# Optimization experiments

Measured on AMD Instinct MI355X. Metric: run time of the kernel, lower is better.

Reference implementation:

```python
import jax, jax.numpy as jnp
import numpy as np

B, S, D_IN, D_HID, D_OUT, H = 2, 2048, 1024, 1024, 1024, 16
HD = D_HID // H  # head_dim = 64


def setup_inputs() -> dict:
    key = jax.random.key(0)
    ks = jax.random.split(key, 9)
    s_in = 1.0 / np.sqrt(D_IN)
    s_out = 1.0 / np.sqrt(D_OUT)
    return {
        "x": jax.random.normal(ks[0], (B, S, D_IN), dtype=jnp.float32),
        "Wq": jax.random.uniform(ks[1], (D_IN, D_HID), jnp.float32, -s_in, s_in),
        "bq": jax.random.uniform(ks[2], (D_HID,), jnp.float32, -s_in, s_in),
        "Wk": jax.random.uniform(ks[3], (D_IN, D_HID), jnp.float32, -s_in, s_in),
        "bk": jax.random.uniform(ks[4], (D_HID,), jnp.float32, -s_in, s_in),
        "Wv": jax.random.uniform(ks[5], (D_IN, D_OUT), jnp.float32, -s_in, s_in),
        "bv": jax.random.uniform(ks[6], (D_OUT,), jnp.float32, -s_in, s_in),
        "Wo": jax.random.uniform(ks[7], (D_OUT, D_OUT), jnp.float32, -s_out, s_out),
        "bo": jax.random.uniform(ks[8], (D_OUT,), jnp.float32, -s_out, s_out),
    }


def reference(x, Wq, bq, Wk, bk, Wv, bv, Wo, bo):
    b, s, _ = x.shape
    q = (x @ Wq + bq).reshape(b, s, H, HD)  # [B,S,H,HD]
    k = (x @ Wk + bk).reshape(b, s, H, HD)
    v = (x @ Wv + bv).reshape(b, s, H, HD)
    scores = jnp.einsum("bqhd,bkhd->bhqk", q, k) / jnp.sqrt(jnp.float32(HD))
    attn = jax.nn.softmax(scores, axis=-1)  # [B,H,S,S]
    ctx = jnp.einsum("bhqk,bkhd->bqhd", attn, v).reshape(b, s, D_HID)
    return ctx @ Wo + bo
```

## Files before the change

### kernel.cpp

```cpp
#include <hip/hip_runtime.h>
#include <stdint.h>

typedef __attribute__((ext_vector_type(8))) short short8v;
typedef __attribute__((ext_vector_type(4))) short short4v;
typedef __attribute__((ext_vector_type(4))) float float4v;
typedef __attribute__((ext_vector_type(4))) unsigned short ushort4v;
typedef __attribute__((ext_vector_type(4))) float floatvec4;
typedef __attribute__((ext_vector_type(2))) unsigned int uint2v;

#define DEVI __device__ __forceinline__

DEVI unsigned short f2bf(float f) {
    unsigned int u = __builtin_bit_cast(unsigned int, f);
    u += 0x7FFFu + ((u >> 16) & 1u);
    return (unsigned short)(u >> 16);
}

DEVI unsigned int pk2bf(float a, float b) {
#if defined(__has_builtin) && __has_builtin(__builtin_amdgcn_cvt_pk_bf16_f32)
    auto r = __builtin_amdgcn_cvt_pk_bf16_f32(a, b);
    unsigned int u;
    __builtin_memcpy(&u, &r, 4);
    return u;
#else
    return (unsigned int)f2bf(a) | ((unsigned int)f2bf(b) << 16);
#endif
}

DEVI float ex2(float x) {
#if defined(__has_builtin) && __has_builtin(__builtin_amdgcn_exp2f)
    return __builtin_amdgcn_exp2f(x);
#else
    return __builtin_exp2f(x);
#endif
}

typedef __attribute__((address_space(1))) void GV;
typedef __attribute__((address_space(3))) void LV;
DEVI void gl2lds16(const void* g, void* l) {
    __builtin_amdgcn_global_load_lds((GV*)g, (LV*)l, 16, 0, 0);
}

__global__ void conv_x_kernel(const float* __restrict__ x, unsigned short* __restrict__ xb) {
    const int i = (blockIdx.x * 256 + threadIdx.x) * 4;
    const floatvec4 v = *(const floatvec4*)&x[i];
    ushort4v o;
#pragma unroll
    for (int r = 0; r < 4; r++) o[r] = f2bf(v[r]);
    *(ushort4v*)&xb[i] = o;
}

__global__ void transpose_w4(const float* __restrict__ W0, const float* __restrict__ W1,
                             const float* __restrict__ W2, const float* __restrict__ W3,
                             unsigned short* __restrict__ D0, unsigned short* __restrict__ D1,
                             unsigned short* __restrict__ D2, unsigned short* __restrict__ D3) {
    __shared__ float t[32][33];
    const int tx = threadIdx.x, ty = threadIdx.y;
    const int bx = blockIdx.x, by = blockIdx.y, z = blockIdx.z;
    const float* W = (z == 0) ? W0 : (z == 1) ? W1 : (z == 2) ? W2 : W3;
    unsigned short* D = (z == 0) ? D0 : (z == 1) ? D1 : (z == 2) ? D2 : D3;
#pragma unroll
    for (int i = 0; i < 4; i++)
        t[ty + i * 8][tx] = W[(size_t)(by * 32 + ty + i * 8) * 1024 + bx * 32 + tx];
    __syncthreads();
#pragma unroll
    for (int i = 0; i < 4; i++)
        D[(size_t)(bx * 32 + ty + i * 8) * 1024 + by * 32 + tx] = f2bf(t[tx][ty + i * 8]);
}

__global__ __launch_bounds__(256, 2) void qkv_gemm(
    const unsigned short* __restrict__ X, const unsigned short* __restrict__ Wt,
    const float* __restrict__ bq, const float* __restrict__ bk, const float* __restrict__ bv,
    unsigned short* __restrict__ qb, unsigned short* __restrict__ kb,
    unsigned short* __restrict__ vtb)
{
    __shared__ __align__(16) unsigned short As[128 * 32];
    __shared__ __align__(16) unsigned short Bs[128 * 32];
    const int tid = threadIdx.x, lane = tid & 63, wv = tid >> 6;
    const int quad = lane >> 4, l16 = lane & 15;
    const int w = blockIdx.x >> 3;
    const int n0 = (blockIdx.x & 7) * 128;
    const int row0 = blockIdx.y * 128;
    const unsigned short* Wsel = Wt + (size_t)w * (1024 * 1024);

    const int srow = lane >> 2;
    const int sg = (lane & 3) ^ ((lane >> 2) & 3) ^ ((lane >> 4) & 3);
    const int scol = sg * 8;
    const int fsw = (l16 & 3) ^ ((l16 >> 2) & 3);
    const int wm = (wv >> 1) * 64, wn = (wv & 1) * 64;

    float4v acc[4][4];
#pragma unroll
    for (int i = 0; i < 4; i++)
#pragma unroll
        for (int j = 0; j < 4; j++) acc[i][j] = (float4v){0.f, 0.f, 0.f, 0.f};

    for (int k0 = 0; k0 < 1024; k0 += 32) {
        __syncthreads();
#pragma unroll
        for (int i = 0; i < 2; i++) {
            const int c = wv * 2 + i;
            gl2lds16(X + (size_t)(row0 + c * 16 + srow) * 1024 + k0 + scol, As + c * 512);
            gl2lds16(Wsel + (size_t)(n0 + c * 16 + srow) * 1024 + k0 + scol, Bs + c * 512);
        }
        __syncthreads();
        short8v a[4], b[4];
#pragma unroll
        for (int mt = 0; mt < 4; mt++)
            a[mt] = *(const short8v*)&As[(wm + mt * 16 + l16) * 32 + ((quad ^ fsw) * 8)];
#pragma unroll
        for (int nt = 0; nt < 4; nt++)
            b[nt] = *(const short8v*)&Bs[(wn + nt * 16 + l16) * 32 + ((quad ^ fsw) * 8)];
#pragma unroll
        for (int mt = 0; mt < 4; mt++)
#pragma unroll
            for (int nt = 0; nt < 4; nt++)
                acc[mt][nt] = __builtin_amdgcn_mfma_f32_16x16x32_bf16(a[mt], b[nt], acc[mt][nt], 0, 0, 0);
    }

    const float* bias = (w == 0) ? bq : (w == 1) ? bk : bv;
    const float scl = (w == 0) ? 0.18033688011112042f : 1.0f;
#pragma unroll
    for (int nt = 0; nt < 4; nt++) {
        const int col = n0 + wn + nt * 16 + l16;
        const float bb = bias[col];
        const int h = col >> 6, hd = col & 63;
#pragma unroll
        for (int mt = 0; mt < 4; mt++) {
            const int tok0 = row0 + wm + mt * 16 + quad * 4;
            const int b_ = tok0 >> 11, s0 = tok0 & 2047;
            if (w == 2) {
                ushort4v pk;
#pragma unroll
                for (int r = 0; r < 4; r++) pk[r] = f2bf(acc[mt][nt][r] + bb);
                *(ushort4v*)&vtb[(((size_t)b_ * 16 + h) * 64 + hd) * 2048 + s0] = pk;
            } else {
                unsigned short* dst = (w == 0) ? qb : kb;
#pragma unroll
                for (int r = 0; r < 4; r++)
                    dst[(((size_t)b_ * 16 + h) * 2048 + (s0 + r)) * 64 + hd] =
                        f2bf((acc[mt][nt][r] + bb) * scl);
            }
        }
    }
}

__global__ __launch_bounds__(256, 4) void attn_kernel(
    const unsigned short* __restrict__ qb, const unsigned short* __restrict__ kb,
    const unsigned short* __restrict__ vtb, unsigned short* __restrict__ ctxb)
{
    __shared__ __align__(16) unsigned short Kt[128 * 64];
    __shared__ __align__(16) unsigned short Vt[64 * 128];
    __shared__ __align__(16) unsigned short Pbs[4][32 * 32];
    const int tid = threadIdx.x, lane = tid & 63, wv = tid >> 6;
    const int quad = lane >> 4, l16 = lane & 15;
    const int bh = blockIdx.x, qt = blockIdx.y;
    const size_t boff = (size_t)bh * (2048 * 64);
    const unsigned short* qp = qb + boff;
    const unsigned short* kp = kb + boff;
    const unsigned short* vp = vtb + boff;
    const int q0 = qt * 128 + wv * 32;

    short8v qf[2][2];
#pragma unroll
    for (int nt = 0; nt < 2; nt++)
#pragma unroll
        for (int kc = 0; kc < 2; kc++)
            qf[nt][kc] = *(const short8v*)&qp[(size_t)(q0 + nt * 16 + l16) * 64 + kc * 32 + quad * 8];

    float4v accO[2][4];
#pragma unroll
    for (int nt = 0; nt < 2; nt++)
#pragma unroll
        for (int ht = 0; ht < 4; ht++) accO[nt][ht] = (float4v){0.f, 0.f, 0.f, 0.f};
    float lsum[2] = {0.f, 0.f};

    const int krow = lane >> 3;
    const int kg = (lane & 7) ^ (lane >> 3);
    const int vrow = lane >> 4;
    const int rsw = l16 & 7;

    const int ktb0 = l16 * 64 + ((quad ^ rsw) * 8);
    const int ktb1 = l16 * 64 + (((4 + quad) ^ rsw) * 8);
    const int vrb = l16 * 128 + ((quad ^ (l16 & 3)) * 8);
    const int l12e = (l16 & 12) * 8;
    const int pwb = l16 * 32 + ((quad ^ ((l16 >> 1) & 3)) * 4);
    const int hsw = (l16 >> 3) & 1;
    const int s1 = (l16 >> 1) & 1;
    const int prbase = l16 * 32 + ((quad ^ ((l16 >> 2) & 3)) * 8);
    const int pr0 = prbase + s1 * 4;
    const int pr1 = prbase + (1 - s1) * 4;

    for (int kt0 = 0; kt0 < 2048; kt0 += 128) {
        __syncthreads();
#pragma unroll
        for (int i = 0; i < 4; i++) {
            const int c = wv * 4 + i;
            gl2lds16(kp + (size_t)(kt0 + c * 8 + krow) * 64 + kg * 8, Kt + c * 512);
            const int vr = c * 4 + vrow;
            const int vg = (lane & 15) ^ (vr & 15);
            gl2lds16(vp + (size_t)vr * 2048 + kt0 + vg * 8, Vt + c * 512);
        }
        __syncthreads();

#pragma unroll
        for (int kc = 0; kc < 4; kc++) {
#pragma unroll
            for (int h = 0; h < 2; h++) {
                const int mt = kc * 2 + h;
                const short8v a0 = *(const short8v*)&Kt[ktb0 + mt * 1024];
                const short8v a1 = *(const short8v*)&Kt[ktb1 + mt * 1024];
                const int hoff = (h ^ hsw) * 16;
#pragma unroll
                for (int nt = 0; nt < 2; nt++) {
                    float4v z = (float4v){0.f, 0.f, 0.f, 0.f};
                    z = __builtin_amdgcn_mfma_f32_16x16x32_bf16(a0, qf[nt][0], z, 0, 0, 0);
                    z = __builtin_amdgcn_mfma_f32_16x16x32_bf16(a1, qf[nt][1], z, 0, 0, 0);
                    const float p0 = ex2(z[0]), p1 = ex2(z[1]);
                    const float p2 = ex2(z[2]), p3 = ex2(z[3]);
                    lsum[nt] += (p0 + p1) + (p2 + p3);
                    *(uint2v*)&Pbs[wv][pwb + hoff + nt * 512] =
                        (uint2v){pk2bf(p0, p1), pk2bf(p2, p3)};
                }
            }
            short8v bvv[4];
            const int roff = (kc * 32) ^ l12e;
#pragma unroll
            for (int ht = 0; ht < 4; ht++)
                bvv[ht] = *(const short8v*)&Vt[vrb + roff + ht * 2048];
            asm volatile("s_waitcnt lgkmcnt(0)" ::: "memory");
#pragma unroll
            for (int nt = 0; nt < 2; nt++) {
                const short4v d0 = *(const short4v*)&Pbs[wv][pr0 + nt * 512];
                const short4v d1 = *(const short4v*)&Pbs[wv][pr1 + nt * 512];
                const short8v ap = __builtin_shufflevector(d0, d1, 0, 1, 2, 3, 4, 5, 6, 7);
#pragma unroll
                for (int ht = 0; ht < 4; ht++)
                    accO[nt][ht] = __builtin_amdgcn_mfma_f32_16x16x32_bf16(ap, bvv[ht], accO[nt][ht], 0, 0, 0);
            }
        }
    }

#pragma unroll
    for (int nt = 0; nt < 2; nt++) {
        lsum[nt] += __shfl_xor(lsum[nt], 16);
        lsum[nt] += __shfl_xor(lsum[nt], 32);
    }

    const int b_ = bh >> 4, h = bh & 15;
#pragma unroll
    for (int nt = 0; nt < 2; nt++)
#pragma unroll
        for (int r = 0; r < 4; r++) {
            const int s = q0 + nt * 16 + quad * 4 + r;
            const float inv = 1.0f / __shfl(lsum[nt], quad * 4 + r);
#pragma unroll
            for (int ht = 0; ht < 4; ht++) {
                const int hd = ht * 16 + l16;
                ctxb[((size_t)(b_ * 2048 + s)) * 1024 + h * 64 + hd] = f2bf(accO[nt][ht][r] * inv);
            }
        }
}

__global__ __launch_bounds__(256, 2) void out_gemm(
    const unsigned short* __restrict__ ctx, const unsigned short* __restrict__ Wot,
    const float* __restrict__ bo, float* __restrict__ out)
{
    __shared__ __align__(16) unsigned short As[128 * 32];
    __shared__ __align__(16) unsigned short Bs[128 * 32];
    const int tid = threadIdx.x, lane = tid & 63, wv = tid >> 6;
    const int quad = lane >> 4, l16 = lane & 15;
    const int n0 = blockIdx.x * 128;
    const int row0 = blockIdx.y * 128;

    const int srow = lane >> 2;
    const int sg = (lane & 3) ^ ((lane >> 2) & 3) ^ ((lane >> 4) & 3);
    const int scol = sg * 8;
    const int fsw = (l16 & 3) ^ ((l16 >> 2) & 3);
    const int wm = (wv >> 1) * 64, wn = (wv & 1) * 64;

    float4v acc[4][4];
#pragma unroll
    for (int i = 0; i < 4; i++)
#pragma unroll
        for (int j = 0; j < 4; j++) acc[i][j] = (float4v){0.f, 0.f, 0.f, 0.f};

    for (int k0 = 0; k0 < 1024; k0 += 32) {
        __syncthreads();
#pragma unroll
        for (int i = 0; i < 2; i++) {
            const int c = wv * 2 + i;
            gl2lds16(ctx + (size_t)(row0 + c * 16 + srow) * 1024 + k0 + scol, As + c * 512);
            gl2lds16(Wot + (size_t)(n0 + c * 16 + srow) * 1024 + k0 + scol, Bs + c * 512);
        }
        __syncthreads();
        short8v a[4], b[4];
#pragma unroll
        for (int mt = 0; mt < 4; mt++)
            a[mt] = *(const short8v*)&As[(wm + mt * 16 + l16) * 32 + ((quad ^ fsw) * 8)];
#pragma unroll
        for (int nt = 0; nt < 4; nt++)
            b[nt] = *(const short8v*)&Bs[(wn + nt * 16 + l16) * 32 + ((quad ^ fsw) * 8)];
#pragma unroll
        for (int mt = 0; mt < 4; mt++)
#pragma unroll
            for (int nt = 0; nt < 4; nt++)
                acc[mt][nt] = __builtin_amdgcn_mfma_f32_16x16x32_bf16(a[mt], b[nt], acc[mt][nt], 0, 0, 0);
    }

#pragma unroll
    for (int nt = 0; nt < 4; nt++) {
        const int col = n0 + wn + nt * 16 + l16;
        const float bb = bo[col];
#pragma unroll
        for (int mt = 0; mt < 4; mt++) {
            const int tok0 = row0 + wm + mt * 16 + quad * 4;
#pragma unroll
            for (int r = 0; r < 4; r++)
                out[(size_t)(tok0 + r) * 1024 + col] = acc[mt][nt][r] + bb;
        }
    }
}

extern "C" void kernel_launch(void* const* d_in, const int* in_sizes, int n_in,
                              void* d_out, int out_size, void* d_ws, size_t ws_size,
                              hipStream_t stream) {
    const float* x  = (const float*)d_in[0];
    const float* Wq = (const float*)d_in[1];
    const float* bq = (const float*)d_in[2];
    const float* Wk = (const float*)d_in[3];
    const float* bk = (const float*)d_in[4];
    const float* Wv = (const float*)d_in[5];
    const float* bv = (const float*)d_in[6];
    const float* Wo = (const float*)d_in[7];
    const float* bo = (const float*)d_in[8];
    float* out = (float*)d_out;

    char* ws = (char*)d_ws;
    unsigned short* xb   = (unsigned short*)(ws);
    unsigned short* qbuf = (unsigned short*)(ws + (8u << 20));
    unsigned short* kbuf = (unsigned short*)(ws + (16u << 20));
    unsigned short* vtb  = (unsigned short*)(ws + (24u << 20));
    unsigned short* wt   = (unsigned short*)(ws + (32u << 20));
    unsigned short* wot  = (unsigned short*)(ws + (38u << 20));

    conv_x_kernel<<<4096, 256, 0, stream>>>(x, xb);
    transpose_w4<<<dim3(32, 32, 4), dim3(32, 8), 0, stream>>>(
        Wq, Wk, Wv, Wo, wt, wt + (1u << 20), wt + (2u << 20), wot);

    qkv_gemm<<<dim3(24, 32), 256, 0, stream>>>(xb, wt, bq, bk, bv, qbuf, kbuf, vtb);
    attn_kernel<<<dim3(32, 16), 256, 0, stream>>>(qbuf, kbuf, vtb, xb );
    out_gemm<<<dim3(8, 32), 256, 0, stream>>>(xb, wot, bo, out);
}
```

Measured before the change: 220.6 us.

## Split attention KV range across two wave groups and shrink out_gemm tiles

```diff
diff --git a/kernel.cpp b/kernel.cpp
--- a/kernel.cpp
+++ b/kernel.cpp
@@ -68,7 +68,7 @@
         D[(size_t)(bx * 32 + ty + i * 8) * 1024 + by * 32 + tx] = f2bf(t[tx][ty + i * 8]);
 }
 
-__global__ __launch_bounds__(256, 2) void qkv_gemm(
+__global__ __launch_bounds__(256, 3) void qkv_gemm(
     const unsigned short* __restrict__ X, const unsigned short* __restrict__ Wt,
     const float* __restrict__ bq, const float* __restrict__ bk, const float* __restrict__ bv,
     unsigned short* __restrict__ qb, unsigned short* __restrict__ kb,
@@ -145,21 +145,22 @@
     }
 }
 
-__global__ __launch_bounds__(256, 4) void attn_kernel(
+__global__ __launch_bounds__(512, 4) void attn_kernel(
     const unsigned short* __restrict__ qb, const unsigned short* __restrict__ kb,
     const unsigned short* __restrict__ vtb, unsigned short* __restrict__ ctxb)
 {
-    __shared__ __align__(16) unsigned short Kt[128 * 64];
-    __shared__ __align__(16) unsigned short Vt[64 * 128];
-    __shared__ __align__(16) unsigned short Pbs[4][32 * 32];
+    __shared__ __align__(16) unsigned short Kt[2][128 * 64];
+    __shared__ __align__(16) unsigned short Vt[2][64 * 128];
+    __shared__ __align__(16) unsigned short Pbs[8][32 * 32];
     const int tid = threadIdx.x, lane = tid & 63, wv = tid >> 6;
+    const int grp = wv >> 2, gw = wv & 3;
     const int quad = lane >> 4, l16 = lane & 15;
     const int bh = blockIdx.x, qt = blockIdx.y;
     const size_t boff = (size_t)bh * (2048 * 64);
     const unsigned short* qp = qb + boff;
     const unsigned short* kp = kb + boff;
     const unsigned short* vp = vtb + boff;
-    const int q0 = qt * 128 + wv * 32;
+    const int q0 = qt * 128 + gw * 32;
 
     short8v qf[2][2];
 #pragma unroll
@@ -191,15 +192,20 @@
     const int pr0 = prbase + s1 * 4;
     const int pr1 = prbase + (1 - s1) * 4;
 
-    for (int kt0 = 0; kt0 < 2048; kt0 += 128) {
+    unsigned short* KtL = Kt[grp];
+    unsigned short* VtL = Vt[grp];
+    const int ktbase = grp * 1024;
+
+    for (int t = 0; t < 8; t++) {
+        const int kt0 = ktbase + t * 128;
         __syncthreads();
 #pragma unroll
         for (int i = 0; i < 4; i++) {
-            const int c = wv * 4 + i;
-            gl2lds16(kp + (size_t)(kt0 + c * 8 + krow) * 64 + kg * 8, Kt + c * 512);
+            const int c = gw * 4 + i;
+            gl2lds16(kp + (size_t)(kt0 + c * 8 + krow) * 64 + kg * 8, KtL + c * 512);
             const int vr = c * 4 + vrow;
             const int vg = (lane & 15) ^ (vr & 15);
-            gl2lds16(vp + (size_t)vr * 2048 + kt0 + vg * 8, Vt + c * 512);
+            gl2lds16(vp + (size_t)vr * 2048 + kt0 + vg * 8, VtL + c * 512);
         }
         __syncthreads();
 
@@ -208,8 +214,8 @@
 #pragma unroll
             for (int h = 0; h < 2; h++) {
                 const int mt = kc * 2 + h;
-                const short8v a0 = *(const short8v*)&Kt[ktb0 + mt * 1024];
-                const short8v a1 = *(const short8v*)&Kt[ktb1 + mt * 1024];
+                const short8v a0 = *(const short8v*)&KtL[ktb0 + mt * 1024];
+                const short8v a1 = *(const short8v*)&KtL[ktb1 + mt * 1024];
                 const int hoff = (h ^ hsw) * 16;
 #pragma unroll
                 for (int nt = 0; nt < 2; nt++) {
@@ -227,7 +233,7 @@
             const int roff = (kc * 32) ^ l12e;
 #pragma unroll
             for (int ht = 0; ht < 4; ht++)
-                bvv[ht] = *(const short8v*)&Vt[vrb + roff + ht * 2048];
+                bvv[ht] = *(const short8v*)&VtL[vrb + roff + ht * 2048];
             asm volatile("s_waitcnt lgkmcnt(0)" ::: "memory");
 #pragma unroll
             for (int nt = 0; nt < 2; nt++) {
@@ -247,62 +253,93 @@
         lsum[nt] += __shfl_xor(lsum[nt], 32);
     }
 
-    const int b_ = bh >> 4, h = bh & 15;
-#pragma unroll
-    for (int nt = 0; nt < 2; nt++)
-#pragma unroll
-        for (int r = 0; r < 4; r++) {
-            const int s = q0 + nt * 16 + quad * 4 + r;
-            const float inv = 1.0f / __shfl(lsum[nt], quad * 4 + r);
-#pragma unroll
-            for (int ht = 0; ht < 4; ht++) {
-                const int hd = ht * 16 + l16;
-                ctxb[((size_t)(b_ * 2048 + s)) * 1024 + h * 64 + hd] = f2bf(accO[nt][ht][r] * inv);
+    __syncthreads();
+    float* Ob = (float*)&Kt[0][0];
+    float* Lb = (float*)&Pbs[0][0];
+    if (grp == 1) {
+        float* dst = Ob + gw * (32 * 68);
+#pragma unroll
+        for (int nt = 0; nt < 2; nt++) {
+#pragma unroll
+            for (int ht = 0; ht < 4; ht++)
+#pragma unroll
+                for (int r = 0; r < 4; r++)
+                    dst[(nt * 16 + quad * 4 + r) * 68 + ht * 16 + l16] = accO[nt][ht][r];
+            if (quad == 0) Lb[gw * 32 + nt * 16 + l16] = lsum[nt];
+        }
+    }
+    __syncthreads();
+    if (grp == 0) {
+        const float* src = Ob + gw * (32 * 68);
+        const int b_ = bh >> 4, h = bh & 15;
+#pragma unroll
+        for (int nt = 0; nt < 2; nt++) {
+            lsum[nt] += Lb[gw * 32 + nt * 16 + l16];
+#pragma unroll
+            for (int ht = 0; ht < 4; ht++)
+#pragma unroll
+                for (int r = 0; r < 4; r++)
+                    accO[nt][ht][r] += src[(nt * 16 + quad * 4 + r) * 68 + ht * 16 + l16];
+        }
+#pragma unroll
+        for (int nt = 0; nt < 2; nt++)
+#pragma unroll
+            for (int r = 0; r < 4; r++) {
+                const int s = q0 + nt * 16 + quad * 4 + r;
+                const float inv = 1.0f / __shfl(lsum[nt], quad * 4 + r);
+#pragma unroll
+                for (int ht = 0; ht < 4; ht++) {
+                    const int hd = ht * 16 + l16;
+                    ctxb[((size_t)(b_ * 2048 + s)) * 1024 + h * 64 + hd] = f2bf(accO[nt][ht][r] * inv);
+                }
             }
-        }
-}
-
-__global__ __launch_bounds__(256, 2) void out_gemm(
+    }
+}
+
+__global__ __launch_bounds__(256, 4) void out_gemm(
     const unsigned short* __restrict__ ctx, const unsigned short* __restrict__ Wot,
     const float* __restrict__ bo, float* __restrict__ out)
 {
-    __shared__ __align__(16) unsigned short As[128 * 32];
+    __shared__ __align__(16) unsigned short As[64 * 32];
     __shared__ __align__(16) unsigned short Bs[128 * 32];
     const int tid = threadIdx.x, lane = tid & 63, wv = tid >> 6;
     const int quad = lane >> 4, l16 = lane & 15;
     const int n0 = blockIdx.x * 128;
-    const int row0 = blockIdx.y * 128;
+    const int row0 = blockIdx.y * 64;
 
     const int srow = lane >> 2;
     const int sg = (lane & 3) ^ ((lane >> 2) & 3) ^ ((lane >> 4) & 3);
     const int scol = sg * 8;
     const int fsw = (l16 & 3) ^ ((l16 >> 2) & 3);
-    const int wm = (wv >> 1) * 64, wn = (wv & 1) * 64;
-
-    float4v acc[4][4];
-#pragma unroll
-    for (int i = 0; i < 4; i++)
+    const int wm = (wv & 1) * 32, wn = (wv >> 1) * 64;
+
+    float4v acc[2][4];
+#pragma unroll
+    for (int i = 0; i < 2; i++)
 #pragma unroll
         for (int j = 0; j < 4; j++) acc[i][j] = (float4v){0.f, 0.f, 0.f, 0.f};
 
     for (int k0 = 0; k0 < 1024; k0 += 32) {
         __syncthreads();
 #pragma unroll
-        for (int i = 0; i < 2; i++) {
-            const int c = wv * 2 + i;
-            gl2lds16(ctx + (size_t)(row0 + c * 16 + srow) * 1024 + k0 + scol, As + c * 512);
-            gl2lds16(Wot + (size_t)(n0 + c * 16 + srow) * 1024 + k0 + scol, Bs + c * 512);
-        }
-        __syncthreads();
-        short8v a[4], b[4];
-#pragma unroll
-        for (int mt = 0; mt < 4; mt++)
+        for (int i = 0; i < 3; i++) {
+            const int idx = wv * 3 + i;
+            if (idx < 4)
+                gl2lds16(ctx + (size_t)(row0 + idx * 16 + srow) * 1024 + k0 + scol, As + idx * 512);
+            else
+                gl2lds16(Wot + (size_t)(n0 + (idx - 4) * 16 + srow) * 1024 + k0 + scol,
+                         Bs + (idx - 4) * 512);
+        }
+        __syncthreads();
+        short8v a[2], b[4];
+#pragma unroll
+        for (int mt = 0; mt < 2; mt++)
             a[mt] = *(const short8v*)&As[(wm + mt * 16 + l16) * 32 + ((quad ^ fsw) * 8)];
 #pragma unroll
         for (int nt = 0; nt < 4; nt++)
             b[nt] = *(const short8v*)&Bs[(wn + nt * 16 + l16) * 32 + ((quad ^ fsw) * 8)];
 #pragma unroll
-        for (int mt = 0; mt < 4; mt++)
+        for (int mt = 0; mt < 2; mt++)
 #pragma unroll
             for (int nt = 0; nt < 4; nt++)
                 acc[mt][nt] = __builtin_amdgcn_mfma_f32_16x16x32_bf16(a[mt], b[nt], acc[mt][nt], 0, 0, 0);
@@ -313,7 +350,7 @@
         const int col = n0 + wn + nt * 16 + l16;
         const float bb = bo[col];
 #pragma unroll
-        for (int mt = 0; mt < 4; mt++) {
+        for (int mt = 0; mt < 2; mt++) {
             const int tok0 = row0 + wm + mt * 16 + quad * 4;
 #pragma unroll
             for (int r = 0; r < 4; r++)
@@ -349,6 +386,6 @@
         Wq, Wk, Wv, Wo, wt, wt + (1u << 20), wt + (2u << 20), wot);
 
     qkv_gemm<<<dim3(24, 32), 256, 0, stream>>>(xb, wt, bq, bk, bv, qbuf, kbuf, vtb);
-    attn_kernel<<<dim3(32, 16), 256, 0, stream>>>(qbuf, kbuf, vtb, xb );
-    out_gemm<<<dim3(8, 32), 256, 0, stream>>>(xb, wot, bo, out);
-}
+    attn_kernel<<<dim3(32, 16), 512, 0, stream>>>(qbuf, kbuf, vtb, xb );
+    out_gemm<<<dim3(8, 64), 256, 0, stream>>>(xb, wot, bo, out);
+}
```

Result: no change. 222.7 us (+1.0%).
